# Kernel tuning notes

Measured on AMD Instinct MI355X. Metric: run time of the kernel, lower is better.

## Reference

```python
import jax, jax.numpy as jnp
import numpy as np

MAX_SEQ = 20          # text-token prefix length (config.max_seq_length)
NUM_HEADS = 12        # == num_spatial_relations
HEAD_DIM = 64         # 768 / 12
QUADRANTS = (1, 2, 4, 7, 8, 9)
NEG = -10000.0

BS, N_FEAT, D = 128, 182, 768   # N_FEAT = 20 text + 150 ocr/obj + 12 decode steps
R_OCR_OBJ = 150


def setup_inputs() -> dict:
    key = jax.random.key(0)
    ks = jax.random.split(key, 8)
    hidden_states = jax.random.normal(ks[0], (BS, N_FEAT, D), dtype=jnp.float32)
    attention_mask = jnp.where(
        jax.random.uniform(ks[1], (BS, 1, 1, N_FEAT)) < 0.9, 0.0, NEG
    ).astype(jnp.float32)
    # binary spatial relation adjacency (bs, R, R, 12)
    spatial_adj_matrix = jax.random.randint(
        ks[2], (BS, R_OCR_OBJ, R_OCR_OBJ, NUM_HEADS), 0, 2
    ).astype(jnp.float32)
    scale = 0.02
    Wq = jax.random.normal(ks[3], (D, D), dtype=jnp.float32) * scale
    Wk = jax.random.normal(ks[4], (D, D), dtype=jnp.float32) * scale
    Wv = jax.random.normal(ks[5], (D, D), dtype=jnp.float32) * scale
    bq = jnp.zeros((D,), jnp.float32)
    bk = jnp.zeros((D,), jnp.float32)
    bv = jnp.zeros((D,), jnp.float32)
    return {
        "hidden_states": hidden_states,
        "attention_mask": attention_mask,
        "spatial_adj_matrix": spatial_adj_matrix,
        "Wq": Wq, "bq": bq, "Wk": Wk, "bk": bk, "Wv": Wv, "bv": bv,
    }


def _spatial_additive_mask(spatial_adj_matrix, num_features, dtype):
    """Builds (bs, heads, N, N) additive mask in {0, -10000}, faithful to the
    sequential ones-fill / adjacency-copy / quadrant-zero / (1-m)*-10000 / permute."""
    bs, R = spatial_adj_matrix.shape[0], spatial_adj_matrix.shape[1]
    S = MAX_SEQ
    m = jnp.ones((bs, num_features, num_features, NUM_HEADS), dtype)
    m = m.at[:, S:S + R, S:S + R, :].set(spatial_adj_matrix.astype(dtype))
    for quad in QUADRANTS:  # num_spatial_relations == num_heads, so all head channels
        if quad == 1:
            m = m.at[:, :S, :S, :].set(0.0)
        elif quad == 2:
            m = m.at[:, :S, S:S + R, :].set(0.0)
        elif quad == 4:
            m = m.at[:, S:S + R, :S, :].set(0.0)
        elif quad == 7:
            m = m.at[:, S + R:, :S, :].set(0.0)
        elif quad == 8:
            m = m.at[:, S + R:, S:S + R, :].set(0.0)
        elif quad == 9:
            m = m.at[:, S + R:, S + R:, :].set(0.0)
    return jnp.transpose((1.0 - m) * NEG, (0, 3, 1, 2))  # (bs, H, N, N)


def _heads(x, bs, n):
    return jnp.transpose(x.reshape(bs, n, NUM_HEADS, HEAD_DIM), (0, 2, 1, 3))


def reference(hidden_states, attention_mask, spatial_adj_matrix,
              Wq, bq, Wk, bk, Wv, bv):
    bs, n, _ = hidden_states.shape
    spatial = _spatial_additive_mask(spatial_adj_matrix, n, hidden_states.dtype)
    # combined additive mask in {0, -10000}; attention_mask broadcasts (bs,1,1,N)
    combined = jnp.minimum(attention_mask, spatial)
    # 1.0 where a query row has at least one attendable key, else 0.0
    entity_probs_mask = (jnp.max(combined, axis=-1, keepdims=True) + 10000.0) / 10000.0

    q = _heads(hidden_states @ Wq.T + bq, bs, n)  # (bs, H, N, d)
    k = _heads(hidden_states @ Wk.T + bk, bs, n)
    v = _heads(hidden_states @ Wv.T + bv, bs, n)

    scores = jnp.einsum('bhqd,bhkd->bhqk', q, k) / 8.0 + combined  # sqrt(64)=8
    probs = jax.nn.softmax(scores, axis=-1) * entity_probs_mask
    ctx = jnp.einsum('bhqk,bhkd->bhqd', probs, v)
    ctx = jnp.transpose(ctx, (0, 2, 1, 3)).reshape(bs, n, NUM_HEADS * HEAD_DIM)
    return ctx
```

## Files before the change

### kernel.cpp

```cpp
#include <hip/hip_runtime.h>
#include <hip/hip_bf16.h>

#define NBS   128
#define NF    182
#define NP    192
#define DMODEL 768
#define NH    12
#define HDIM  64
#define SEQT  20
#define ROCR  150

typedef __attribute__((ext_vector_type(4))) float  f32x4;
typedef __attribute__((ext_vector_type(8))) short  s16x8;
typedef __attribute__((ext_vector_type(4))) unsigned int u32x4;
using bf16 = __hip_bfloat16;

#define SB()    __builtin_amdgcn_sched_barrier(0)
#define BAR()   __builtin_amdgcn_s_barrier()

__device__ __forceinline__ void gload_lds16(const void* g, void* l) {
    auto gp = (const __attribute__((address_space(1))) unsigned int*)((unsigned long long)g);
    auto lp = (__attribute__((address_space(3))) unsigned int*)(unsigned int)((unsigned long long)l);
    __builtin_amdgcn_global_load_lds(gp, lp, 16, 0, 0);
}

__global__ __launch_bounds__(256) void convert_bf16(
    const float* __restrict__ hs,
    const float* __restrict__ Wq, const float* __restrict__ Wk, const float* __restrict__ Wv,
    bf16* __restrict__ hsb, bf16* __restrict__ Wb2)
{
    const size_t HT = (size_t)NBS * NF * DMODEL / 8;
    const size_t WT = 3ull * DMODEL * DMODEL / 8;
    size_t i = (size_t)blockIdx.x * 256 + threadIdx.x;
    if (i >= HT + WT) return;
    const float* src; bf16* dst;
    if (i < HT) {
        size_t e = i * 8; src = hs + e; dst = hsb + e;
    } else {
        size_t e = (i - HT) * 8;
        int R = (int)(e / DMODEL), c = (int)(e % DMODEL);
        int h = R / 192, t2 = (R % 192) / 64, r0 = R % 64;
        src = (t2 == 0 ? Wq : t2 == 1 ? Wk : Wv) + (size_t)(h * 64 + r0) * DMODEL + c;
        dst = Wb2 + e;
    }
    float4 a = *reinterpret_cast<const float4*>(src);
    float4 b = *reinterpret_cast<const float4*>(src + 4);
    union { s16x8 v; bf16 h8[8]; } u;
    u.h8[0] = __float2bfloat16(a.x); u.h8[1] = __float2bfloat16(a.y);
    u.h8[2] = __float2bfloat16(a.z); u.h8[3] = __float2bfloat16(a.w);
    u.h8[4] = __float2bfloat16(b.x); u.h8[5] = __float2bfloat16(b.y);
    u.h8[6] = __float2bfloat16(b.z); u.h8[7] = __float2bfloat16(b.w);
    *reinterpret_cast<s16x8*>(dst) = u.v;
}

__global__ __launch_bounds__(256) void pack_adj(const float* __restrict__ adj,
                                                unsigned long long* __restrict__ bits)
{
    __shared__ float tile[ROCR * NH];
    const int b = blockIdx.y, r = blockIdx.x;
    const int tid = threadIdx.x, lane = tid & 63, w = tid >> 6;
    const float* src = adj + ((size_t)b * ROCR + r) * (ROCR * NH);
    for (int i = tid; i < ROCR * NH; i += 256) tile[i] = src[i];
    __syncthreads();
    for (int c = w; c < NH * 3; c += 4) {
        int hh = c / 3, wd = c - hh * 3;
        int k = wd * 64 + lane;
        int j = k - SEQT;
        bool v = false;
        if (j >= 0 && j < ROCR) v = (tile[j * NH + hh] > 0.5f);
        unsigned long long m = __ballot(v);
        if (lane == 0) bits[(((size_t)b * NH + hh) * ROCR + r) * 3 + wd] = m;
    }
}

#define KO2   0
#define VTO2  24576
#define QO2   49152
#define LWO2  73728
#define AWO2  78336

__global__ __launch_bounds__(256, 2) void fused_qkv_attn(
    const bf16* __restrict__ hsb, const bf16* __restrict__ Wb2,
    const float* __restrict__ bq, const float* __restrict__ bk, const float* __restrict__ bv,
    const float* __restrict__ amask,
    const unsigned long long* __restrict__ bits,
    float* __restrict__ out)
{
    __shared__ char L[78368];
    const int tid  = threadIdx.x;
    const int lane = tid & 63;
    const int wid  = tid >> 6;
    const int wr = wid >> 1, wc = wid & 1;
    const int lm = lane & 15, lg = lane >> 4;

    const int flat = blockIdx.x;
    const int wgid = (flat & 7) * 192 + (flat >> 3);
    const int b = wgid / NH, h = wgid - b * NH;

    float* obase = out + (size_t)b * NF * DMODEL + h * HDIM;

    if (wid == 0) {
        #pragma unroll
        for (int w = 0; w < 3; ++w) {
            int k = w * 64 + lane;
            bool v = (k < NF) && (amask[b * NF + k] == 0.0f);
            unsigned long long m = __ballot(v);
            if (lane == 0) ((unsigned long long*)(L + AWO2))[w] = m;
        }
    }
    for (int i = tid; i < 12 * 64; i += 256)
        obase[(size_t)(170 + (i >> 6)) * DMODEL + (i & 63)] = 0.f;
    __syncthreads();
    if (tid < NP) {
        int r = tid;
        unsigned long long s0 = 0, s1 = 0, s2 = 0;
        const unsigned long long DEC = 0xFFFull << 42;
        if (r < SEQT) {
            s2 = DEC;
        } else if (r < SEQT + ROCR) {
            const unsigned long long* bp = bits + (((size_t)b * NH + h) * ROCR + (r - SEQT)) * 3;
            s0 = bp[0]; s1 = bp[1]; s2 = bp[2] | DEC;
        }
        unsigned long long* aw = (unsigned long long*)(L + AWO2);
        unsigned long long* Lw = (unsigned long long*)(L + LWO2);
        Lw[r * 3 + 0] = s0 & aw[0];
        Lw[r * 3 + 1] = s1 & aw[1];
        Lw[r * 3 + 2] = s2 & aw[2];
    }

    const char* gA = (const char*)(hsb + (size_t)b * NF * DMODEL);
    const char* gW = (const char*)(Wb2 + (size_t)h * 192 * DMODEL);

    f32x4 acc[6][6];
    #pragma unroll
    for (int i = 0; i < 6; ++i)
        #pragma unroll
        for (int j = 0; j < 6; ++j) acc[i][j] = (f32x4){0.f, 0.f, 0.f, 0.f};

    const int srow4 = tid >> 2, sch4 = tid & 3;

    auto ST = [&](int kt, int bsel) {
        char* dA = L + bsel * 24576;
        char* dW = dA + 12288;
        #pragma unroll
        for (int it = 0; it < 3; ++it) {
            int row = it * 64 + srow4;
            int lc = sch4 ^ ((row >> 1) & 3);
            size_t go = (size_t)row * 1536 + (size_t)kt * 64 + lc * 16;
            int o = row * 64 + sch4 * 16;
            gload_lds16(gA + go, dA + o);
            gload_lds16(gW + go, dW + o);
        }
    };
    auto CP = [&](int bsel) {
        const char* Ab = L + bsel * 24576;
        const char* Wp = Ab + 12288;
        s16x8 af[6], bf6[6];
        #pragma unroll
        for (int mi = 0; mi < 6; ++mi) {
            int r = 96 * wr + 16 * mi + lm;
            af[mi] = *reinterpret_cast<const s16x8*>(Ab + r * 64 + ((lg ^ ((r >> 1) & 3)) << 4));
        }
        #pragma unroll
        for (int ni = 0; ni < 6; ++ni) {
            int r = 96 * wc + 16 * ni + lm;
            bf6[ni] = *reinterpret_cast<const s16x8*>(Wp + r * 64 + ((lg ^ ((r >> 1) & 3)) << 4));
        }
        __builtin_amdgcn_s_setprio(1);
        #pragma unroll
        for (int mi = 0; mi < 6; ++mi)
            #pragma unroll
            for (int ni = 0; ni < 6; ++ni)
                acc[mi][ni] = __builtin_amdgcn_mfma_f32_16x16x32_bf16(af[mi], bf6[ni], acc[mi][ni], 0, 0, 0);
        __builtin_amdgcn_s_setprio(0);
    };

    ST(0, 0);
    ST(1, 1);
    for (int t = 0; t < 24; ++t) {
        if (t < 23) { asm volatile("s_waitcnt vmcnt(6)" ::: "memory"); }
        else        { asm volatile("s_waitcnt vmcnt(0)" ::: "memory"); }
        SB(); BAR(); SB();
        CP(t & 1);
        SB(); BAR();
        if (t + 2 < 24) ST(t + 2, t & 1);
    }
    BAR();

    float bias6[6];
    #pragma unroll
    for (int ni = 0; ni < 6; ++ni) {
        int c = 96 * wc + 16 * ni + lm;
        int whichc = c >> 6, cc = c & 63;
        const float* bp = (whichc == 0) ? bq : (whichc == 1) ? bk : bv;
        bias6[ni] = bp[h * 64 + cc];
    }
    #pragma unroll
    for (int mi = 0; mi < 6; ++mi) {
        #pragma unroll
        for (int ni = 0; ni < 6; ++ni) {
            int c = 96 * wc + 16 * ni + lm;
            #pragma unroll
            for (int j = 0; j < 4; ++j) {
                int row = 96 * wr + 16 * mi + 4 * lg + j;
                bf16 hv = __float2bfloat16(acc[mi][ni][j] + bias6[ni]);
                unsigned short us = *reinterpret_cast<unsigned short*>(&hv);
                if (c < 64) {
                    *reinterpret_cast<unsigned short*>(L + QO2 + row * 128 + ((2 * c) ^ ((row & 7) << 4))) = us;
                } else if (c < 128) {
                    int cc = c - 64;
                    *reinterpret_cast<unsigned short*>(L + KO2 + row * 128 + ((2 * cc) ^ ((row & 7) << 4))) = us;
                } else if (row < NF) {
                    int d = c - 128;
                    *reinterpret_cast<unsigned short*>(L + VTO2 + d * 384 + ((2 * row) ^ ((d & 7) << 4))) = us;
                }
            }
        }
    }
    for (int i = tid; i < 64 * 10; i += 256) {
        int d = i / 10, k2 = NF + (i - d * 10);
        *reinterpret_cast<unsigned short*>(L + VTO2 + d * 384 + ((2 * k2) ^ ((d & 7) << 4))) = 0;
    }
    __syncthreads();

    s16x8 qf[3][2];
    #pragma unroll
    for (int bi = 0; bi < 3; ++bi) {
        int band = wid + 4 * bi;
        int qrow = ((band < 11) ? band : 0) * 16 + lm;
        const char* qb = L + QO2 + qrow * 128;
        int sq = (qrow & 7) << 4;
        qf[bi][0] = *reinterpret_cast<const s16x8*>(qb + ((lg * 16) ^ sq));
        qf[bi][1] = *reinterpret_cast<const s16x8*>(qb + ((64 + lg * 16) ^ sq));
    }
    __syncthreads();

    const unsigned long long* LwA = (const unsigned long long*)(L + LWO2);

    #pragma unroll
    for (int bi = 0; bi < 3; ++bi) {
        const int band = wid + 4 * bi;
        if (band >= 11) continue;
        const int q0 = band * 16;

        const unsigned long long* lwp = LwA + (q0 + lm) * 3;
        unsigned long long mw0 = lwp[0], mw1 = lwp[1], mw2 = lwp[2];

        f32x4 sacc[12];
        #pragma unroll
        for (int t = 0; t < 12; ++t) sacc[t] = (f32x4){0.f, 0.f, 0.f, 0.f};
        #pragma unroll
        for (int t = 0; t < 12; ++t) {
            int key = t * 16 + lm;
            const char* kb = L + KO2 + key * 128;
            int sw = (key & 7) << 4;
            s16x8 kf0 = *reinterpret_cast<const s16x8*>(kb + ((lg * 16) ^ sw));
            s16x8 kf1 = *reinterpret_cast<const s16x8*>(kb + ((64 + lg * 16) ^ sw));
            sacc[t] = __builtin_amdgcn_mfma_f32_16x16x32_bf16(kf0, qf[bi][0], sacc[t], 0, 0, 0);
            sacc[t] = __builtin_amdgcn_mfma_f32_16x16x32_bf16(kf1, qf[bi][1], sacc[t], 0, 0, 0);
        }

        float mx = -3.0e38f;
        #pragma unroll
        for (int t = 0; t < 12; ++t) {
            unsigned long long w = (t < 4) ? mw0 : (t < 8) ? mw1 : mw2;
            #pragma unroll
            for (int j = 0; j < 4; ++j) {
                int sh = ((t & 3) << 4) + 4 * lg + j;
                float s = sacc[t][j] * 0.125f;
                s = ((w >> sh) & 1ull) ? s : -3.0e38f;
                sacc[t][j] = s;
                mx = fmaxf(mx, s);
            }
        }
        mx = fmaxf(mx, __shfl_xor(mx, 16));
        mx = fmaxf(mx, __shfl_xor(mx, 32));
        float sum = 0.f;
        #pragma unroll
        for (int t = 0; t < 12; ++t)
            #pragma unroll
            for (int j = 0; j < 4; ++j) {
                float e = (sacc[t][j] > -1.0e37f) ? __expf(sacc[t][j] - mx) : 0.f;
                sacc[t][j] = e;
                sum += e;
            }
        sum += __shfl_xor(sum, 16);
        sum += __shfl_xor(sum, 32);
        float scl = (mx > -1.0e37f) ? 1.0f / sum : 0.f;

        unsigned int p0[12], p1[12];
        #pragma unroll
        for (int t = 0; t < 12; ++t) {
            bf16 b0 = __float2bfloat16(sacc[t][0] * scl);
            bf16 b1 = __float2bfloat16(sacc[t][1] * scl);
            bf16 b2 = __float2bfloat16(sacc[t][2] * scl);
            bf16 b3 = __float2bfloat16(sacc[t][3] * scl);
            p0[t] = (unsigned int)*reinterpret_cast<unsigned short*>(&b0)
                  | ((unsigned int)*reinterpret_cast<unsigned short*>(&b1) << 16);
            p1[t] = (unsigned int)*reinterpret_cast<unsigned short*>(&b2)
                  | ((unsigned int)*reinterpret_cast<unsigned short*>(&b3) << 16);
        }

        f32x4 oacc[4];
        #pragma unroll
        for (int t = 0; t < 4; ++t) oacc[t] = (f32x4){0.f, 0.f, 0.f, 0.f};
        const bool hi = (lg & 1);
        #pragma unroll
        for (int ks = 0; ks < 6; ++ks) {
            unsigned int A0 = p0[2 * ks],     A1 = p1[2 * ks];
            unsigned int B0 = p0[2 * ks + 1], B1 = p1[2 * ks + 1];
            unsigned int u0 = __shfl_xor(A0, 16), u1 = __shfl_xor(A1, 16);
            unsigned int v0 = __shfl_xor(B0, 16), v1 = __shfl_xor(B1, 16);
            unsigned int hA0 = hi ? u0 : A0, hA1 = hi ? u1 : A1;
            unsigned int hA2 = hi ? A0 : u0, hA3 = hi ? A1 : u1;
            unsigned int hB0 = hi ? v0 : B0, hB1 = hi ? v1 : B1;
            unsigned int hB2 = hi ? B0 : v0, hB3 = hi ? B1 : v1;
            unsigned int xA0 = __shfl_xor(hA0, 32), xA1 = __shfl_xor(hA1, 32);
            unsigned int xA2 = __shfl_xor(hA2, 32), xA3 = __shfl_xor(hA3, 32);
            unsigned int xB0 = __shfl_xor(hB0, 32), xB1 = __shfl_xor(hB1, 32);
            unsigned int xB2 = __shfl_xor(hB2, 32), xB3 = __shfl_xor(hB3, 32);
            u32x4 f;
            if (lg == 0)      f = (u32x4){hA0, hA1, hA2, hA3};
            else if (lg == 1) f = (u32x4){xA0, xA1, xA2, xA3};
            else if (lg == 2) f = (u32x4){xB0, xB1, xB2, xB3};
            else              f = (u32x4){hB0, hB1, hB2, hB3};
            s16x8 pa;
            __builtin_memcpy(&pa, &f, 16);
            #pragma unroll
            for (int t2 = 0; t2 < 4; ++t2) {
                int d = t2 * 16 + lm;
                s16x8 vf = *reinterpret_cast<const s16x8*>(L + VTO2 + d * 384 + ((ks * 64 + lg * 16) ^ ((d & 7) << 4)));
                oacc[t2] = __builtin_amdgcn_mfma_f32_16x16x32_bf16(pa, vf, oacc[t2], 0, 0, 0);
            }
        }
        #pragma unroll
        for (int j = 0; j < 4; ++j) {
            int row = q0 + lg * 4 + j;
            if (row < 170) {
                #pragma unroll
                for (int t2 = 0; t2 < 4; ++t2)
                    obase[(size_t)row * DMODEL + t2 * 16 + lm] = oacc[t2][j];
            }
        }
    }
}

extern "C" void kernel_launch(void* const* d_in, const int* in_sizes, int n_in,
                              void* d_out, int out_size, void* d_ws, size_t ws_size,
                              hipStream_t stream)
{
    const float* hs    = (const float*)d_in[0];
    const float* amask = (const float*)d_in[1];
    const float* adj   = (const float*)d_in[2];
    const float* Wq    = (const float*)d_in[3];
    const float* bq    = (const float*)d_in[4];
    const float* Wk    = (const float*)d_in[5];
    const float* bk    = (const float*)d_in[6];
    const float* Wv    = (const float*)d_in[7];
    const float* bv    = (const float*)d_in[8];
    float* out = (float*)d_out;

    char* ws = (char*)d_ws;
    bf16* Wb2 = (bf16*)ws;
    unsigned long long* bits = (unsigned long long*)(ws + 3538944);
    bf16* hsb = (bf16*)(ws + 3538944 + 5529600);

    const int cvt_blocks = (int)(((size_t)NBS * NF * DMODEL / 8 + 3ull * DMODEL * DMODEL / 8 + 255) / 256);
    convert_bf16<<<cvt_blocks, 256, 0, stream>>>(hs, Wq, Wk, Wv, hsb, Wb2);
    pack_adj<<<dim3(ROCR, NBS), 256, 0, stream>>>(adj, bits);
    fused_qkv_attn<<<dim3(NBS * NH), 256, 0, stream>>>(hsb, Wb2, bq, bk, bv, amask, bits, out);
}
```

Before: 222.1 us.

## Spill Q tile to global scratch to fit three workgroups per CU; merge prep kernels

The Q projection output is written to a global scratch buffer instead of LDS, and each wave reads its Q fragments back from global. This shrinks shared memory from about 78KB to about 53KB so launch bounds can go from 2 to 3 blocks per CU. The bf16 conversion and adjacency bit-packing kernels are merged into one launch to save a kernel launch. The cost is extra global traffic for Q and possibly more register pressure under the tighter launch bound.

Result: slower. 552.7 us (+148.9%).

```diff
diff --git a/kernel.cpp b/kernel.cpp
--- a/kernel.cpp
+++ b/kernel.cpp
@@ -24,69 +24,71 @@
     __builtin_amdgcn_global_load_lds(gp, lp, 16, 0, 0);
 }
 
-__global__ __launch_bounds__(256) void convert_bf16(
+#define CVT_BLOCKS 9600
+__global__ __launch_bounds__(256) void prep(
     const float* __restrict__ hs,
     const float* __restrict__ Wq, const float* __restrict__ Wk, const float* __restrict__ Wv,
-    bf16* __restrict__ hsb, bf16* __restrict__ Wb2)
-{
-    const size_t HT = (size_t)NBS * NF * DMODEL / 8;
-    const size_t WT = 3ull * DMODEL * DMODEL / 8;
-    size_t i = (size_t)blockIdx.x * 256 + threadIdx.x;
-    if (i >= HT + WT) return;
-    const float* src; bf16* dst;
-    if (i < HT) {
-        size_t e = i * 8; src = hs + e; dst = hsb + e;
-    } else {
-        size_t e = (i - HT) * 8;
-        int R = (int)(e / DMODEL), c = (int)(e % DMODEL);
-        int h = R / 192, t2 = (R % 192) / 64, r0 = R % 64;
-        src = (t2 == 0 ? Wq : t2 == 1 ? Wk : Wv) + (size_t)(h * 64 + r0) * DMODEL + c;
-        dst = Wb2 + e;
-    }
-    float4 a = *reinterpret_cast<const float4*>(src);
-    float4 b = *reinterpret_cast<const float4*>(src + 4);
-    union { s16x8 v; bf16 h8[8]; } u;
-    u.h8[0] = __float2bfloat16(a.x); u.h8[1] = __float2bfloat16(a.y);
-    u.h8[2] = __float2bfloat16(a.z); u.h8[3] = __float2bfloat16(a.w);
-    u.h8[4] = __float2bfloat16(b.x); u.h8[5] = __float2bfloat16(b.y);
-    u.h8[6] = __float2bfloat16(b.z); u.h8[7] = __float2bfloat16(b.w);
-    *reinterpret_cast<s16x8*>(dst) = u.v;
-}
-
-__global__ __launch_bounds__(256) void pack_adj(const float* __restrict__ adj,
-                                                unsigned long long* __restrict__ bits)
+    const float* __restrict__ adj,
+    bf16* __restrict__ hsb, bf16* __restrict__ Wb2,
+    unsigned long long* __restrict__ bits)
 {
     __shared__ float tile[ROCR * NH];
-    const int b = blockIdx.y, r = blockIdx.x;
-    const int tid = threadIdx.x, lane = tid & 63, w = tid >> 6;
-    const float* src = adj + ((size_t)b * ROCR + r) * (ROCR * NH);
-    for (int i = tid; i < ROCR * NH; i += 256) tile[i] = src[i];
-    __syncthreads();
-    for (int c = w; c < NH * 3; c += 4) {
-        int hh = c / 3, wd = c - hh * 3;
-        int k = wd * 64 + lane;
-        int j = k - SEQT;
-        bool v = false;
-        if (j >= 0 && j < ROCR) v = (tile[j * NH + hh] > 0.5f);
-        unsigned long long m = __ballot(v);
-        if (lane == 0) bits[(((size_t)b * NH + hh) * ROCR + r) * 3 + wd] = m;
+    if (blockIdx.x < CVT_BLOCKS) {
+        const size_t HT = (size_t)NBS * NF * DMODEL / 8;
+        const size_t WT = 3ull * DMODEL * DMODEL / 8;
+        size_t i = (size_t)blockIdx.x * 256 + threadIdx.x;
+        if (i >= HT + WT) return;
+        const float* src; bf16* dst;
+        if (i < HT) {
+            size_t e = i * 8; src = hs + e; dst = hsb + e;
+        } else {
+            size_t e = (i - HT) * 8;
+            int R = (int)(e / DMODEL), c = (int)(e % DMODEL);
+            int h = R / 192, t2 = (R % 192) / 64, r0 = R % 64;
+            src = (t2 == 0 ? Wq : t2 == 1 ? Wk : Wv) + (size_t)(h * 64 + r0) * DMODEL + c;
+            dst = Wb2 + e;
+        }
+        float4 a = *reinterpret_cast<const float4*>(src);
+        float4 b = *reinterpret_cast<const float4*>(src + 4);
+        union { s16x8 v; bf16 h8[8]; } u;
+        u.h8[0] = __float2bfloat16(a.x); u.h8[1] = __float2bfloat16(a.y);
+        u.h8[2] = __float2bfloat16(a.z); u.h8[3] = __float2bfloat16(a.w);
+        u.h8[4] = __float2bfloat16(b.x); u.h8[5] = __float2bfloat16(b.y);
+        u.h8[6] = __float2bfloat16(b.z); u.h8[7] = __float2bfloat16(b.w);
+        *reinterpret_cast<s16x8*>(dst) = u.v;
+    } else {
+        const int pb = blockIdx.x - CVT_BLOCKS;
+        const int b = pb / ROCR, r = pb - b * ROCR;
+        const int tid = threadIdx.x, lane = tid & 63, w = tid >> 6;
+        const float* src = adj + ((size_t)b * ROCR + r) * (ROCR * NH);
+        for (int i = tid; i < ROCR * NH; i += 256) tile[i] = src[i];
+        __syncthreads();
+        for (int c = w; c < NH * 3; c += 4) {
+            int hh = c / 3, wd = c - hh * 3;
+            int k = wd * 64 + lane;
+            int j = k - SEQT;
+            bool v = false;
+            if (j >= 0 && j < ROCR) v = (tile[j * NH + hh] > 0.5f);
+            unsigned long long m = __ballot(v);
+            if (lane == 0) bits[(((size_t)b * NH + hh) * ROCR + r) * 3 + wd] = m;
+        }
     }
 }
 
 #define KO2   0
 #define VTO2  24576
-#define QO2   49152
-#define LWO2  73728
-#define AWO2  78336
-
-__global__ __launch_bounds__(256, 2) void fused_qkv_attn(
+#define LWO2  49152
+#define AWO2  53376
+
+__global__ __launch_bounds__(256, 3) void fused_qkv_attn(
     const bf16* __restrict__ hsb, const bf16* __restrict__ Wb2,
     const float* __restrict__ bq, const float* __restrict__ bk, const float* __restrict__ bv,
     const float* __restrict__ amask,
     const unsigned long long* __restrict__ bits,
+    bf16* __restrict__ qg,
     float* __restrict__ out)
 {
-    __shared__ char L[78368];
+    __shared__ char L[53400];
     const int tid  = threadIdx.x;
     const int lane = tid & 63;
     const int wid  = tid >> 6;
@@ -98,6 +100,7 @@
     const int b = wgid / NH, h = wgid - b * NH;
 
     float* obase = out + (size_t)b * NF * DMODEL + h * HDIM;
+    bf16*  qgb   = qg + (size_t)wgid * (176 * 64);
 
     if (wid == 0) {
         #pragma unroll
@@ -111,7 +114,7 @@
     for (int i = tid; i < 12 * 64; i += 256)
         obase[(size_t)(170 + (i >> 6)) * DMODEL + (i & 63)] = 0.f;
     __syncthreads();
-    if (tid < NP) {
+    if (tid < 176) {
         int r = tid;
         unsigned long long s0 = 0, s1 = 0, s2 = 0;
         const unsigned long long DEC = 0xFFFull << 42;
@@ -206,7 +209,7 @@
                 bf16 hv = __float2bfloat16(acc[mi][ni][j] + bias6[ni]);
                 unsigned short us = *reinterpret_cast<unsigned short*>(&hv);
                 if (c < 64) {
-                    *reinterpret_cast<unsigned short*>(L + QO2 + row * 128 + ((2 * c) ^ ((row & 7) << 4))) = us;
+                    if (row < 176) qgb[row * 64 + c] = hv;
                 } else if (c < 128) {
                     int cc = c - 64;
                     *reinterpret_cast<unsigned short*>(L + KO2 + row * 128 + ((2 * cc) ^ ((row & 7) << 4))) = us;
@@ -227,13 +230,11 @@
     #pragma unroll
     for (int bi = 0; bi < 3; ++bi) {
         int band = wid + 4 * bi;
-        int qrow = ((band < 11) ? band : 0) * 16 + lm;
-        const char* qb = L + QO2 + qrow * 128;
-        int sq = (qrow & 7) << 4;
-        qf[bi][0] = *reinterpret_cast<const s16x8*>(qb + ((lg * 16) ^ sq));
-        qf[bi][1] = *reinterpret_cast<const s16x8*>(qb + ((64 + lg * 16) ^ sq));
-    }
-    __syncthreads();
+        int qrow = ((band < 11) ? band * 16 : 0) + lm;
+        const bf16* qb = qgb + qrow * 64;
+        qf[bi][0] = *reinterpret_cast<const s16x8*>(qb + lg * 8);
+        qf[bi][1] = *reinterpret_cast<const s16x8*>(qb + 32 + lg * 8);
+    }
 
     const unsigned long long* LwA = (const unsigned long long*)(L + LWO2);
 
@@ -364,9 +365,8 @@
     bf16* Wb2 = (bf16*)ws;
     unsigned long long* bits = (unsigned long long*)(ws + 3538944);
     bf16* hsb = (bf16*)(ws + 3538944 + 5529600);
-
-    const int cvt_blocks = (int)(((size_t)NBS * NF * DMODEL / 8 + 3ull * DMODEL * DMODEL / 8 + 255) / 256);
-    convert_bf16<<<cvt_blocks, 256, 0, stream>>>(hs, Wq, Wk, Wv, hsb, Wb2);
-    pack_adj<<<dim3(ROCR, NBS), 256, 0, stream>>>(adj, bits);
-    fused_qkv_attn<<<dim3(NBS * NH), 256, 0, stream>>>(hsb, Wb2, bq, bk, bv, amask, bits, out);
+    bf16* qg  = (bf16*)(ws + 3538944 + 5529600 + 35782656);
+
+    prep<<<dim3(CVT_BLOCKS + ROCR * NBS), 256, 0, stream>>>(hs, Wq, Wk, Wv, adj, hsb, Wb2, bits);
+    fused_qkv_attn<<<dim3(NBS * NH), 256, 0, stream>>>(hsb, Wb2, bq, bk, bv, amask, bits, qg, out);
 }
```
